# Kernel optimization log

Measured on AMD Instinct MI355X. Metric: run time of the kernel, lower is better.

## Reference

```python
import jax, jax.numpy as jnp
import numpy as np

D_MODEL = 1024
NUM_HEADS = 16
D_K = D_MODEL // NUM_HEADS
THETA = 10000.0
B, S = 2, 2048


def apply_rope(x, token_position, theta=THETA):
    # x: [B, H, S, d_k]; token_position: [B, S] int
    d_k = x.shape[-1]
    inv_freq = 1.0 / theta ** (jnp.arange(0, d_k, 2, dtype=jnp.float32) / d_k)  # [d_k/2]
    angles = token_position.astype(jnp.float32)[:, :, None] * inv_freq[None, None, :]  # [B,S,d_k/2]
    cos = jnp.cos(angles)[:, None, :, :]  # [B,1,S,d_k/2]
    sin = jnp.sin(angles)[:, None, :, :]
    x_even = x[..., 0::2]
    x_odd = x[..., 1::2]
    rot_even = x_even * cos - x_odd * sin
    rot_odd = x_even * sin + x_odd * cos
    # interleave back: stack on new last axis, then flatten
    return jnp.stack([rot_even, rot_odd], axis=-1).reshape(x.shape)


def setup_inputs() -> dict:
    key = jax.random.key(0)
    kx, kq, kk, kv, ko = jax.random.split(key, 5)
    scale = 1.0 / np.sqrt(D_MODEL)
    x = jax.random.normal(kx, (B, S, D_MODEL), dtype=jnp.float32)
    WQ = jax.random.normal(kq, (D_MODEL, D_MODEL), dtype=jnp.float32) * scale
    WK = jax.random.normal(kk, (D_MODEL, D_MODEL), dtype=jnp.float32) * scale
    WV = jax.random.normal(kv, (D_MODEL, D_MODEL), dtype=jnp.float32) * scale
    WO = jax.random.normal(ko, (D_MODEL, D_MODEL), dtype=jnp.float32) * scale
    token_position = jnp.broadcast_to(jnp.arange(S, dtype=jnp.int32)[None, :], (B, S))
    return {"x": x, "token_position": token_position, "WQ": WQ, "WK": WK, "WV": WV, "WO": WO}


def reference(x, token_position, WQ, WK, WV, WO):
    Batch, seq, _ = x.shape
    Q = jnp.einsum('bsd,de->bse', x, WQ).reshape(Batch, seq, NUM_HEADS, D_K).transpose(0, 2, 1, 3)
    K = jnp.einsum('bsd,de->bse', x, WK).reshape(Batch, seq, NUM_HEADS, D_K).transpose(0, 2, 1, 3)
    V = jnp.einsum('bsd,de->bse', x, WV).reshape(Batch, seq, NUM_HEADS, D_K).transpose(0, 2, 1, 3)
    Q = apply_rope(Q, token_position)
    K = apply_rope(K, token_position)
    score = jnp.einsum('bhqd,bhkd->bhqk', Q, K) / jnp.sqrt(jnp.float32(D_K))
    causal = jnp.tril(jnp.ones((seq, seq), dtype=bool))  # [S,S]
    score = jnp.where(causal[None, None, :, :], score, -jnp.inf)
    probs = jax.nn.softmax(score, axis=-1)
    out = jnp.einsum('bhqk,bhkd->bhqd', probs, V)
    out = out.transpose(0, 2, 1, 3).reshape(Batch, seq, D_MODEL)
    return jnp.einsum('bsd,de->bse', out, WO)
```

## Files before the change

kernel.cpp:

```cpp
#include <hip/hip_runtime.h>
#include <hip/hip_bf16.h>

typedef __attribute__((ext_vector_type(8))) short short8;
typedef __attribute__((ext_vector_type(4))) float f32x4;
typedef __hip_bfloat16 bf16_t;

#define SEQ 2048
#define DM 1024
#define NH 16
#define DK 64
#define NKT 16

static __device__ __forceinline__ f32x4 mfma16x16x32(short8 a, short8 b, f32x4 c) {
  return __builtin_amdgcn_mfma_f32_16x16x32_bf16(a, b, c, 0, 0, 0);
}

typedef const __attribute__((address_space(1))) unsigned int ga_u32_t;
typedef __attribute__((address_space(3))) unsigned int lds_u32_t;
static __device__ __forceinline__ void gld16(const bf16_t* g, bf16_t* l) {
  __builtin_amdgcn_global_load_lds((ga_u32_t*)g, (lds_u32_t*)l, 16, 0, 0);
}
static __device__ __forceinline__ void bar() { asm volatile("s_barrier" ::: "memory"); }
static __device__ __forceinline__ void wait_vm8() { asm volatile("s_waitcnt vmcnt(8)" ::: "memory"); }
static __device__ __forceinline__ void wait_vm0() { asm volatile("s_waitcnt vmcnt(0)" ::: "memory"); }

static __device__ __forceinline__ void stage_tile(const bf16_t* asrc, const bf16_t* bsrc,
                                                  char* bufbase, int w, int kk) {
#pragma unroll
  for (int j = 0; j < 4; ++j) {
    gld16(asrc + (size_t)(j * 32) * DM + kk, (bf16_t*)(bufbase + j * 4096 + w * 1024));
    gld16(bsrc + (size_t)(j * 32) * DM + kk, (bf16_t*)(bufbase + 16384 + j * 4096 + w * 1024));
  }
}

__global__ void sniff_dtype(const unsigned int* __restrict__ x, int* __restrict__ flag) {
  int lane = threadIdx.x & 63;
  int cnt = 0;
  for (int r = 0; r < 4; ++r) {
    unsigned int v = x[lane + r * 64];
    int e = (v >> 7) & 0xFF;
    if (e >= 100 && e <= 145) cnt++;
  }
  for (int d = 1; d < 64; d <<= 1) cnt += __shfl_xor(cnt, d, 64);
  if (lane == 0) *flag = (cnt >= 192) ? 1 : 0;
}

__global__ __launch_bounds__(256) void prep(const void* __restrict__ x,
                                            bf16_t* __restrict__ Xc,
                                            const void* __restrict__ w0,
                                            const void* __restrict__ w1,
                                            const void* __restrict__ w2,
                                            const void* __restrict__ w3,
                                            bf16_t* __restrict__ wt_base,
                                            const int* __restrict__ tokpos,
                                            float2* __restrict__ rtab,
                                            const int* __restrict__ flag) {
  int f = *flag;
  int bx = blockIdx.x, t = threadIdx.x;
  __shared__ bf16_t tile[64][65];
  if (bx < 4096) {
    int i = bx * 256 + t;
    if (f) {
      ((uint2*)Xc)[i] = ((const uint2*)x)[i];
    } else {
      const float4 v = ((const float4*)x)[i];
      bf16_t o[4] = {__float2bfloat16(v.x), __float2bfloat16(v.y),
                     __float2bfloat16(v.z), __float2bfloat16(v.w)};
      ((uint2*)Xc)[i] = *(const uint2*)o;
    }
  } else if (bx < 5120) {
    int rem = bx - 4096;
    int z = rem >> 8, bxx = rem & 15, byy = (rem >> 4) & 15;
    const void* src = (z == 0) ? w0 : (z == 1) ? w1 : (z == 2) ? w2 : w3;
    bf16_t* dst = wt_base + (size_t)((z + 1) & 3) * DM * DM;
    int tx = t & 63, ty = t >> 6;
    int r0 = byy * 64, c0 = bxx * 64;
    for (int i = 0; i < 64; i += 4) {
      size_t idx = (size_t)(r0 + ty + i) * DM + c0 + tx;
      tile[ty + i][tx] = f ? ((const bf16_t*)src)[idx]
                           : __float2bfloat16(((const float*)src)[idx]);
    }
    __syncthreads();
    for (int i = 0; i < 64; i += 4)
      dst[(size_t)(c0 + ty + i) * DM + r0 + tx] = tile[tx][ty + i];
  } else {
    int i = (bx - 5120) * 256 + t;
    int m = i >> 5, pp = i & 31;
    float pos = (float)tokpos[m];
    float invf = __powf(10000.0f, -(float)pp * (1.0f / 32.0f));
    float sn, cs;
    sincosf(pos * invf, &sn, &cs);
    rtab[i] = make_float2(cs, sn);
  }
}

__global__ __launch_bounds__(256) void gemm128_qkv(const bf16_t* __restrict__ A,
                                                   const bf16_t* __restrict__ WTqkv,
                                                   bf16_t* __restrict__ Qb,
                                                   bf16_t* __restrict__ Kb,
                                                   bf16_t* __restrict__ VTo,
                                                   const float2* __restrict__ rtab) {
  __shared__ __align__(16) char smem[65536];
  int t = threadIdx.x;
  int w = t >> 6, lane = t & 63, l15 = lane & 15, quad = lane >> 4;
  int wrow = w >> 1, wcol = w & 1;
  int m0 = blockIdx.y * 128, nx = blockIdx.x, n0 = nx * 128;
  int srow0 = w * 8 + (lane >> 3);
  int scg = (lane & 7) ^ (lane >> 3);
  const bf16_t* asrc = A + (size_t)(m0 + srow0) * DM + scg * 8;
  const bf16_t* bsrc = WTqkv + (size_t)(n0 + srow0) * DM + scg * 8;

  f32x4 acc[4][4] = {};
  stage_tile(asrc, bsrc, smem, w, 0);
  stage_tile(asrc, bsrc, smem + 32768, w, 64);
  for (int kt = 0; kt < NKT; ++kt) {
    if (kt < NKT - 1) wait_vm8(); else wait_vm0();
    bar();
    const bf16_t* Ab = (const bf16_t*)(smem + (kt & 1) * 32768);
    const bf16_t* Bb = Ab + 8192;
    short8 af[4][2], bfr[4][2];
#pragma unroll
    for (int mt = 0; mt < 4; ++mt) {
      int r = wrow * 64 + mt * 16 + l15;
      af[mt][0] = *(const short8*)(Ab + r * 64 + ((quad ^ (l15 & 7)) * 8));
      af[mt][1] = *(const short8*)(Ab + r * 64 + (((4 + quad) ^ (l15 & 7)) * 8));
    }
#pragma unroll
    for (int nt = 0; nt < 4; ++nt) {
      int r = wcol * 64 + nt * 16 + l15;
      bfr[nt][0] = *(const short8*)(Bb + r * 64 + ((quad ^ (l15 & 7)) * 8));
      bfr[nt][1] = *(const short8*)(Bb + r * 64 + (((4 + quad) ^ (l15 & 7)) * 8));
    }
#pragma unroll
    for (int mt = 0; mt < 4; ++mt)
#pragma unroll
      for (int nt = 0; nt < 4; ++nt) {
        acc[mt][nt] = mfma16x16x32(af[mt][0], bfr[nt][0], acc[mt][nt]);
        acc[mt][nt] = mfma16x16x32(af[mt][1], bfr[nt][1], acc[mt][nt]);
      }
    bar();
    if (kt + 2 < NKT)
      stage_tile(asrc, bsrc, smem + (kt & 1) * 32768, w, (kt + 2) * 64);
  }

  int sel = nx >> 3;
  int nc = (nx & 7) * 128;
  __syncthreads();
  bf16_t (*Tw)[72] = (bf16_t(*)[72])(smem + w * 9216);
  int b = m0 >> 11;
  int h = (nc >> 6) + wcol;
  if (sel < 2) {
    bf16_t* dst = sel ? Kb : Qb;
    float sgnv = (l15 & 1) ? 1.0f : -1.0f;
#pragma unroll
    for (int mt = 0; mt < 4; ++mt)
#pragma unroll
      for (int r = 0; r < 4; ++r) {
        int m = m0 + wrow * 64 + mt * 16 + quad * 4 + r;
        const float2* tr = rtab + m * 32;
#pragma unroll
        for (int nt = 0; nt < 4; ++nt) {
          int d = nt * 16 + l15;
          float val = acc[mt][nt][r];
          float partner = __shfl_xor(val, 1, 64);
          float2 cssn = tr[d >> 1];
          Tw[mt * 16 + quad * 4 + r][d] = __float2bfloat16(val * cssn.x + sgnv * partner * cssn.y);
        }
      }
    int s_base = (m0 & (SEQ - 1)) + wrow * 64;
    bf16_t* dq = dst + ((size_t)(b * NH + h) * SEQ + s_base) * DK;
#pragma unroll
    for (int c = 0; c < 8; ++c) {
      int row = c * 8 + (lane >> 3);
      int col = (lane & 7) * 8;
      *(short8*)&dq[(size_t)row * DK + col] = *(const short8*)&Tw[row][col];
    }
  } else {
#pragma unroll
    for (int mt = 0; mt < 4; ++mt)
#pragma unroll
      for (int nt = 0; nt < 4; ++nt)
#pragma unroll
        for (int r = 0; r < 4; ++r)
          Tw[nt * 16 + l15][mt * 16 + quad * 4 + r] = __float2bfloat16(acc[mt][nt][r]);
    int s_base = m0 & (SEQ - 1);
#pragma unroll
    for (int c = 0; c < 4; ++c) {
      int d = c * 16 + (lane >> 2);
      int s2 = (lane & 3) * 16;
      size_t ob = ((size_t)(b * NH + h) * DK + d) * SEQ + s_base + wrow * 64 + s2;
      *(short8*)&VTo[ob] = *(const short8*)&Tw[d][s2];
      *(short8*)&VTo[ob + 8] = *(const short8*)&Tw[d][s2 + 8];
    }
  }
}

__global__ __launch_bounds__(256) void gemm128_out(const bf16_t* __restrict__ A,
                                                   const bf16_t* __restrict__ BT,
                                                   void* __restrict__ out,
                                                   const int* __restrict__ flag) {
  __shared__ __align__(16) char smem[65536];
  int f = *flag;
  int t = threadIdx.x;
  int w = t >> 6, lane = t & 63, l15 = lane & 15, quad = lane >> 4;
  int wrow = w >> 1, wcol = w & 1;
  int m0 = blockIdx.y * 128, n0 = blockIdx.x * 128;
  int srow0 = w * 8 + (lane >> 3);
  int scg = (lane & 7) ^ (lane >> 3);
  const bf16_t* asrc = A + (size_t)(m0 + srow0) * DM + scg * 8;
  const bf16_t* bsrc = BT + (size_t)(n0 + srow0) * DM + scg * 8;

  f32x4 acc[4][4] = {};
  stage_tile(asrc, bsrc, smem, w, 0);
  stage_tile(asrc, bsrc, smem + 32768, w, 64);
  for (int kt = 0; kt < NKT; ++kt) {
    if (kt < NKT - 1) wait_vm8(); else wait_vm0();
    bar();
    const bf16_t* Ab = (const bf16_t*)(smem + (kt & 1) * 32768);
    const bf16_t* Bb = Ab + 8192;
    short8 af[4][2], bfr[4][2];
#pragma unroll
    for (int mt = 0; mt < 4; ++mt) {
      int r = wrow * 64 + mt * 16 + l15;
      af[mt][0] = *(const short8*)(Ab + r * 64 + ((quad ^ (l15 & 7)) * 8));
      af[mt][1] = *(const short8*)(Ab + r * 64 + (((4 + quad) ^ (l15 & 7)) * 8));
    }
#pragma unroll
    for (int nt = 0; nt < 4; ++nt) {
      int r = wcol * 64 + nt * 16 + l15;
      bfr[nt][0] = *(const short8*)(Bb + r * 64 + ((quad ^ (l15 & 7)) * 8));
      bfr[nt][1] = *(const short8*)(Bb + r * 64 + (((4 + quad) ^ (l15 & 7)) * 8));
    }
#pragma unroll
    for (int mt = 0; mt < 4; ++mt)
#pragma unroll
      for (int nt = 0; nt < 4; ++nt) {
        acc[mt][nt] = mfma16x16x32(af[mt][0], bfr[nt][0], acc[mt][nt]);
        acc[mt][nt] = mfma16x16x32(af[mt][1], bfr[nt][1], acc[mt][nt]);
      }
    bar();
    if (kt + 2 < NKT)
      stage_tile(asrc, bsrc, smem + (kt & 1) * 32768, w, (kt + 2) * 64);
  }
#pragma unroll
  for (int mt = 0; mt < 4; ++mt)
#pragma unroll
    for (int nt = 0; nt < 4; ++nt)
#pragma unroll
      for (int r = 0; r < 4; ++r) {
        int m = m0 + wrow * 64 + mt * 16 + quad * 4 + r;
        int col = n0 + wcol * 64 + nt * 16 + l15;
        size_t oidx = (size_t)m * DM + col;
        if (f) ((bf16_t*)out)[oidx] = __float2bfloat16(acc[mt][nt][r]);
        else   ((float*)out)[oidx] = acc[mt][nt][r];
      }
}

__global__ __launch_bounds__(256) void attn_fwd(const bf16_t* __restrict__ Q,
                                                const bf16_t* __restrict__ K,
                                                const bf16_t* __restrict__ VT,
                                                bf16_t* __restrict__ O) {
  int x = blockIdx.x, bh = blockIdx.y;
  int b = bh >> 4, h = bh & 15;
  int g = x + (bh << 4);
  int raw = (g + (g >> 8)) & 15;
  const int pmap[16] = {0, 15, 1, 13, 2, 12, 3, 11, 4, 10, 5, 9, 6, 8, 7, 14};
  int p = pmap[raw];
  int qA = p, qB = 31 - p;
  int t = threadIdx.x;
  int w = t >> 6, lane = t & 63, l15 = lane & 15, quad = lane >> 4;
  const size_t base = (size_t)bh * SEQ * DK;
  const bf16_t* Qp = Q + base;
  const bf16_t* Kp = K + base;
  const bf16_t* VTp = VT + base;

  __shared__ __align__(16) bf16_t Ks[64][72];
  __shared__ __align__(16) bf16_t Vs[64][72];
  __shared__ __align__(16) bf16_t Pb[4][2][16][72];

  int rowA = qA * 64 + w * 16 + l15;
  int rowB = qB * 64 + w * 16 + l15;
  short8 qfA0 = *(const short8*)(Qp + (size_t)rowA * DK + quad * 8);
  short8 qfA1 = *(const short8*)(Qp + (size_t)rowA * DK + 32 + quad * 8);
  short8 qfB0 = *(const short8*)(Qp + (size_t)rowB * DK + quad * 8);
  short8 qfB1 = *(const short8*)(Qp + (size_t)rowB * DK + 32 + quad * 8);

  int srow = t >> 2, scoff = (t & 3) * 16;
  const bf16_t* kst = Kp + (size_t)srow * DK + scoff;
  const bf16_t* vst = VTp + (size_t)srow * SEQ + scoff;

  short8 kA = *(const short8*)(kst);
  short8 kB = *(const short8*)(kst + 8);
  short8 vA = *(const short8*)(vst);
  short8 vB = *(const short8*)(vst + 8);

  f32x4 oA[4] = {}, oB[4] = {};
  float rA[4] = {0.f, 0.f, 0.f, 0.f}, rB[4] = {0.f, 0.f, 0.f, 0.f};

  for (int kb = 0; kb <= qB; ++kb) {
    __syncthreads();
    *(short8*)&Ks[srow][scoff] = kA;
    *(short8*)&Ks[srow][scoff + 8] = kB;
    *(short8*)&Vs[srow][scoff] = vA;
    *(short8*)&Vs[srow][scoff + 8] = vB;
    __syncthreads();

    int nkb = (kb < qB) ? (kb + 1) : qB;
    kA = *(const short8*)(kst + (size_t)nkb * 64 * DK);
    kB = *(const short8*)(kst + (size_t)nkb * 64 * DK + 8);
    vA = *(const short8*)(vst + (size_t)nkb * 64);
    vB = *(const short8*)(vst + (size_t)nkb * 64 + 8);

    bool doA = (kb <= qA);

    {
      f32x4 sc[4];
#pragma unroll
      for (int kt = 0; kt < 4; ++kt) {
        f32x4 a = {};
        a = mfma16x16x32(qfB0, *(const short8*)&Ks[kt * 16 + l15][quad * 8], a);
        a = mfma16x16x32(qfB1, *(const short8*)&Ks[kt * 16 + l15][32 + quad * 8], a);
        sc[kt] = a;
      }
      bool diag = (kb == qB);
#pragma unroll
      for (int kt = 0; kt < 4; ++kt)
#pragma unroll
        for (int reg = 0; reg < 4; ++reg) {
          float sv = sc[kt][reg] * 0.125f;
          if (diag) {
            int kg = kt * 16 + l15, qg = w * 16 + quad * 4 + reg;
            if (kg > qg) sv = -30000.0f;
          }
          float pp = __expf(sv);
          rB[reg] += pp;
          Pb[w][1][quad * 4 + reg][kt * 16 + l15] = __float2bfloat16(pp);
        }
      short8 p0 = *(const short8*)&Pb[w][1][l15][quad * 8];
      short8 p1 = *(const short8*)&Pb[w][1][l15][32 + quad * 8];
#pragma unroll
      for (int dt = 0; dt < 4; ++dt) {
        oB[dt] = mfma16x16x32(p0, *(const short8*)&Vs[dt * 16 + l15][quad * 8], oB[dt]);
        oB[dt] = mfma16x16x32(p1, *(const short8*)&Vs[dt * 16 + l15][32 + quad * 8], oB[dt]);
      }
    }
    if (doA) {
      f32x4 sc[4];
#pragma unroll
      for (int kt = 0; kt < 4; ++kt) {
        f32x4 a = {};
        a = mfma16x16x32(qfA0, *(const short8*)&Ks[kt * 16 + l15][quad * 8], a);
        a = mfma16x16x32(qfA1, *(const short8*)&Ks[kt * 16 + l15][32 + quad * 8], a);
        sc[kt] = a;
      }
      bool diag = (kb == qA);
#pragma unroll
      for (int kt = 0; kt < 4; ++kt)
#pragma unroll
        for (int reg = 0; reg < 4; ++reg) {
          float sv = sc[kt][reg] * 0.125f;
          if (diag) {
            int kg = kt * 16 + l15, qg = w * 16 + quad * 4 + reg;
            if (kg > qg) sv = -30000.0f;
          }
          float pp = __expf(sv);
          rA[reg] += pp;
          Pb[w][0][quad * 4 + reg][kt * 16 + l15] = __float2bfloat16(pp);
        }
      short8 p0 = *(const short8*)&Pb[w][0][l15][quad * 8];
      short8 p1 = *(const short8*)&Pb[w][0][l15][32 + quad * 8];
#pragma unroll
      for (int dt = 0; dt < 4; ++dt) {
        oA[dt] = mfma16x16x32(p0, *(const short8*)&Vs[dt * 16 + l15][quad * 8], oA[dt]);
        oA[dt] = mfma16x16x32(p1, *(const short8*)&Vs[dt * 16 + l15][32 + quad * 8], oA[dt]);
      }
    }
  }

  for (int d = 1; d < 16; d <<= 1)
#pragma unroll
    for (int reg = 0; reg < 4; ++reg) {
      rA[reg] += __shfl_xor(rA[reg], d, 64);
      rB[reg] += __shfl_xor(rB[reg], d, 64);
    }

#pragma unroll
  for (int dt = 0; dt < 4; ++dt)
#pragma unroll
    for (int reg = 0; reg < 4; ++reg) {
      int col = h * DK + dt * 16 + l15;
      int qa = qA * 64 + w * 16 + quad * 4 + reg;
      int qb_ = qB * 64 + w * 16 + quad * 4 + reg;
      O[((size_t)b * SEQ + qa) * DM + col] = __float2bfloat16(oA[dt][reg] / rA[reg]);
      O[((size_t)b * SEQ + qb_) * DM + col] = __float2bfloat16(oB[dt][reg] / rB[reg]);
    }
}

extern "C" void kernel_launch(void* const* d_in, const int* in_sizes, int n_in,
                              void* d_out, int out_size, void* d_ws, size_t ws_size,
                              hipStream_t stream) {
  const void* x = d_in[0];
  const int* tokpos = (const int*)d_in[1];
  const void* WQ = d_in[2];
  const void* WK = d_in[3];
  const void* WV = d_in[4];
  const void* WO = d_in[5];

  char* ws = (char*)d_ws;
  const size_t MB = 1024 * 1024;
  bf16_t* WT  = (bf16_t*)ws;
  bf16_t* Xc  = (bf16_t*)(ws + 8 * MB);
  bf16_t* Qb  = (bf16_t*)(ws + 16 * MB);
  bf16_t* Kb  = (bf16_t*)(ws + 24 * MB);
  bf16_t* VTb = (bf16_t*)(ws + 32 * MB);
  bf16_t* Ab  = (bf16_t*)(ws + 8 * MB);
  int* flag   = (int*)(ws + 40 * MB);
  float2* rtab = (float2*)(ws + 41 * MB);

  dim3 blk(256);
  sniff_dtype<<<1, 64, 0, stream>>>((const unsigned int*)x, flag);
  prep<<<5632, blk, 0, stream>>>(x, Xc, WQ, WK, WV, WO, WT, tokpos, rtab, flag);
  gemm128_qkv<<<dim3(24, 32), blk, 0, stream>>>(Xc, WT + (size_t)DM * DM, Qb, Kb, VTb, rtab);
  attn_fwd<<<dim3(16, 32), blk, 0, stream>>>(Qb, Kb, VTb, Ab);
  gemm128_out<<<dim3(8, 32), blk, 0, stream>>>(Ab, WT, d_out, flag);
}
```

Baseline: 185.8 us.

## Split attention KV loop across two wave groups and reduce partials in LDS

Doubles the attention block to 512 threads, with two groups of four waves each handling alternating key blocks (even/odd) for the same query tiles, each group using its own K/V LDS buffers. Partial outputs and row sums from group 1 are written to shared memory and added by group 0 before normalisation and store. This aims to halve the serial KV loop length per block and raise wave-level parallelism. The cost is more LDS (72KB), extra barriers and a final reduction, plus possible idle waves when the count of key blocks is odd.

```diff
diff --git a/kernel.cpp b/kernel.cpp
--- a/kernel.cpp
+++ b/kernel.cpp
@@ -256,70 +256,81 @@
       }
 }
 
-__global__ __launch_bounds__(256) void attn_fwd(const bf16_t* __restrict__ Q,
+__global__ __launch_bounds__(512) void attn_fwd(const bf16_t* __restrict__ Q,
                                                 const bf16_t* __restrict__ K,
                                                 const bf16_t* __restrict__ VT,
                                                 bf16_t* __restrict__ O) {
   int x = blockIdx.x, bh = blockIdx.y;
   int b = bh >> 4, h = bh & 15;
-  int g = x + (bh << 4);
-  int raw = (g + (g >> 8)) & 15;
+  int g4 = x + (bh << 4);
+  int raw = (g4 + (g4 >> 8)) & 15;
   const int pmap[16] = {0, 15, 1, 13, 2, 12, 3, 11, 4, 10, 5, 9, 6, 8, 7, 14};
   int p = pmap[raw];
   int qA = p, qB = 31 - p;
   int t = threadIdx.x;
   int w = t >> 6, lane = t & 63, l15 = lane & 15, quad = lane >> 4;
+  int g = w >> 2;
+  int wq = w & 3;
   const size_t base = (size_t)bh * SEQ * DK;
   const bf16_t* Qp = Q + base;
   const bf16_t* Kp = K + base;
   const bf16_t* VTp = VT + base;
 
-  __shared__ __align__(16) bf16_t Ks[64][72];
-  __shared__ __align__(16) bf16_t Vs[64][72];
-  __shared__ __align__(16) bf16_t Pb[4][2][16][72];
-
-  int rowA = qA * 64 + w * 16 + l15;
-  int rowB = qB * 64 + w * 16 + l15;
+  __shared__ __align__(16) char smem[73728];
+  bf16_t (*Ks)[64][72] = (bf16_t(*)[64][72])smem;
+  bf16_t (*Vs)[64][72] = (bf16_t(*)[64][72])(smem + 18432);
+  bf16_t (*Pb)[2][16][72] = (bf16_t(*)[2][16][72])(smem + 36864);
+
+  int rowA = qA * 64 + wq * 16 + l15;
+  int rowB = qB * 64 + wq * 16 + l15;
   short8 qfA0 = *(const short8*)(Qp + (size_t)rowA * DK + quad * 8);
   short8 qfA1 = *(const short8*)(Qp + (size_t)rowA * DK + 32 + quad * 8);
   short8 qfB0 = *(const short8*)(Qp + (size_t)rowB * DK + quad * 8);
   short8 qfB1 = *(const short8*)(Qp + (size_t)rowB * DK + 32 + quad * 8);
 
-  int srow = t >> 2, scoff = (t & 3) * 16;
+  int tl = t & 255;
+  int srow = tl >> 2, scoff = (tl & 3) * 16;
   const bf16_t* kst = Kp + (size_t)srow * DK + scoff;
   const bf16_t* vst = VTp + (size_t)srow * SEQ + scoff;
 
-  short8 kA = *(const short8*)(kst);
-  short8 kB = *(const short8*)(kst + 8);
-  short8 vA = *(const short8*)(vst);
-  short8 vB = *(const short8*)(vst + 8);
+  short8 kA = *(const short8*)(kst + (size_t)g * 64 * DK);
+  short8 kB = *(const short8*)(kst + (size_t)g * 64 * DK + 8);
+  short8 vA = *(const short8*)(vst + (size_t)g * 64);
+  short8 vB = *(const short8*)(vst + (size_t)g * 64 + 8);
 
   f32x4 oA[4] = {}, oB[4] = {};
   float rA[4] = {0.f, 0.f, 0.f, 0.f}, rB[4] = {0.f, 0.f, 0.f, 0.f};
 
-  for (int kb = 0; kb <= qB; ++kb) {
+  int ni = qB / 2 + 1;
+  for (int i = 0; i < ni; ++i) {
+    int kb = 2 * i + g;
+    bool active = (kb <= qB);
     __syncthreads();
-    *(short8*)&Ks[srow][scoff] = kA;
-    *(short8*)&Ks[srow][scoff + 8] = kB;
-    *(short8*)&Vs[srow][scoff] = vA;
-    *(short8*)&Vs[srow][scoff + 8] = vB;
+    if (active) {
+      *(short8*)&Ks[g][srow][scoff] = kA;
+      *(short8*)&Ks[g][srow][scoff + 8] = kB;
+      *(short8*)&Vs[g][srow][scoff] = vA;
+      *(short8*)&Vs[g][srow][scoff + 8] = vB;
+    }
     __syncthreads();
 
-    int nkb = (kb < qB) ? (kb + 1) : qB;
-    kA = *(const short8*)(kst + (size_t)nkb * 64 * DK);
-    kB = *(const short8*)(kst + (size_t)nkb * 64 * DK + 8);
-    vA = *(const short8*)(vst + (size_t)nkb * 64);
-    vB = *(const short8*)(vst + (size_t)nkb * 64 + 8);
+    int nkb = (kb + 2 <= qB) ? (kb + 2) : kb;
+    if (active) {
+      kA = *(const short8*)(kst + (size_t)nkb * 64 * DK);
+      kB = *(const short8*)(kst + (size_t)nkb * 64 * DK + 8);
+      vA = *(const short8*)(vst + (size_t)nkb * 64);
+      vB = *(const short8*)(vst + (size_t)nkb * 64 + 8);
+    }
+    if (!active) continue;
 
     bool doA = (kb <= qA);
-
     {
       f32x4 sc[4];
 #pragma unroll
       for (int kt = 0; kt < 4; ++kt) {
         f32x4 a = {};
-        a = mfma16x16x32(qfB0, *(const short8*)&Ks[kt * 16 + l15][quad * 8], a);
-        a = mfma16x16x32(qfB1, *(const short8*)&Ks[kt * 16 + l15][32 + quad * 8], a);
+        a = mfma16x16x32(qfB0, *(const short8*)&Ks[g][kt * 16 + l15][quad * 8], a);
+        a = mfma16x16x32(qfB1, *(const short8*)&Ks[g][kt * 16 + l15][32 + quad * 8], a);
         sc[kt] = a;
       }
       bool diag = (kb == qB);
@@ -329,7 +340,7 @@
         for (int reg = 0; reg < 4; ++reg) {
           float sv = sc[kt][reg] * 0.125f;
           if (diag) {
-            int kg = kt * 16 + l15, qg = w * 16 + quad * 4 + reg;
+            int kg = kt * 16 + l15, qg = wq * 16 + quad * 4 + reg;
             if (kg > qg) sv = -30000.0f;
           }
           float pp = __expf(sv);
@@ -340,8 +351,8 @@
       short8 p1 = *(const short8*)&Pb[w][1][l15][32 + quad * 8];
 #pragma unroll
       for (int dt = 0; dt < 4; ++dt) {
-        oB[dt] = mfma16x16x32(p0, *(const short8*)&Vs[dt * 16 + l15][quad * 8], oB[dt]);
-        oB[dt] = mfma16x16x32(p1, *(const short8*)&Vs[dt * 16 + l15][32 + quad * 8], oB[dt]);
+        oB[dt] = mfma16x16x32(p0, *(const short8*)&Vs[g][dt * 16 + l15][quad * 8], oB[dt]);
+        oB[dt] = mfma16x16x32(p1, *(const short8*)&Vs[g][dt * 16 + l15][32 + quad * 8], oB[dt]);
       }
     }
     if (doA) {
@@ -349,8 +360,8 @@
 #pragma unroll
       for (int kt = 0; kt < 4; ++kt) {
         f32x4 a = {};
-        a = mfma16x16x32(qfA0, *(const short8*)&Ks[kt * 16 + l15][quad * 8], a);
-        a = mfma16x16x32(qfA1, *(const short8*)&Ks[kt * 16 + l15][32 + quad * 8], a);
+        a = mfma16x16x32(qfA0, *(const short8*)&Ks[g][kt * 16 + l15][quad * 8], a);
+        a = mfma16x16x32(qfA1, *(const short8*)&Ks[g][kt * 16 + l15][32 + quad * 8], a);
         sc[kt] = a;
       }
       bool diag = (kb == qA);
@@ -360,7 +371,7 @@
         for (int reg = 0; reg < 4; ++reg) {
           float sv = sc[kt][reg] * 0.125f;
           if (diag) {
-            int kg = kt * 16 + l15, qg = w * 16 + quad * 4 + reg;
+            int kg = kt * 16 + l15, qg = wq * 16 + quad * 4 + reg;
             if (kg > qg) sv = -30000.0f;
           }
           float pp = __expf(sv);
@@ -371,8 +382,8 @@
       short8 p1 = *(const short8*)&Pb[w][0][l15][32 + quad * 8];
 #pragma unroll
       for (int dt = 0; dt < 4; ++dt) {
-        oA[dt] = mfma16x16x32(p0, *(const short8*)&Vs[dt * 16 + l15][quad * 8], oA[dt]);
-        oA[dt] = mfma16x16x32(p1, *(const short8*)&Vs[dt * 16 + l15][32 + quad * 8], oA[dt]);
+        oA[dt] = mfma16x16x32(p0, *(const short8*)&Vs[g][dt * 16 + l15][quad * 8], oA[dt]);
+        oA[dt] = mfma16x16x32(p1, *(const short8*)&Vs[g][dt * 16 + l15][32 + quad * 8], oA[dt]);
       }
     }
   }
@@ -384,16 +395,51 @@
       rB[reg] += __shfl_xor(rB[reg], d, 64);
     }
 
-#pragma unroll
-  for (int dt = 0; dt < 4; ++dt)
+  float (*OcA)[16][68] = (float(*)[16][68])smem;
+  float (*OcB)[16][68] = (float(*)[16][68])(smem + 17408);
+  float (*RcA)[16] = (float(*)[16])(smem + 34816);
+  float (*RcB)[16] = (float(*)[16])(smem + 35072);
+  __syncthreads();
+  if (g == 1) {
+#pragma unroll
+    for (int dt = 0; dt < 4; ++dt)
+#pragma unroll
+      for (int reg = 0; reg < 4; ++reg) {
+        OcA[wq][quad * 4 + reg][dt * 16 + l15] = oA[dt][reg];
+        OcB[wq][quad * 4 + reg][dt * 16 + l15] = oB[dt][reg];
+      }
+    if (l15 == 0)
+#pragma unroll
+      for (int reg = 0; reg < 4; ++reg) {
+        RcA[wq][quad * 4 + reg] = rA[reg];
+        RcB[wq][quad * 4 + reg] = rB[reg];
+      }
+  }
+  __syncthreads();
+  if (g == 0) {
+#pragma unroll
+    for (int dt = 0; dt < 4; ++dt)
+#pragma unroll
+      for (int reg = 0; reg < 4; ++reg) {
+        oA[dt][reg] += OcA[wq][quad * 4 + reg][dt * 16 + l15];
+        oB[dt][reg] += OcB[wq][quad * 4 + reg][dt * 16 + l15];
+      }
 #pragma unroll
     for (int reg = 0; reg < 4; ++reg) {
-      int col = h * DK + dt * 16 + l15;
-      int qa = qA * 64 + w * 16 + quad * 4 + reg;
-      int qb_ = qB * 64 + w * 16 + quad * 4 + reg;
-      O[((size_t)b * SEQ + qa) * DM + col] = __float2bfloat16(oA[dt][reg] / rA[reg]);
-      O[((size_t)b * SEQ + qb_) * DM + col] = __float2bfloat16(oB[dt][reg] / rB[reg]);
-    }
+      rA[reg] += RcA[wq][quad * 4 + reg];
+      rB[reg] += RcB[wq][quad * 4 + reg];
+    }
+#pragma unroll
+    for (int dt = 0; dt < 4; ++dt)
+#pragma unroll
+      for (int reg = 0; reg < 4; ++reg) {
+        int col = h * DK + dt * 16 + l15;
+        int qa = qA * 64 + wq * 16 + quad * 4 + reg;
+        int qb_ = qB * 64 + wq * 16 + quad * 4 + reg;
+        O[((size_t)b * SEQ + qa) * DM + col] = __float2bfloat16(oA[dt][reg] / rA[reg]);
+        O[((size_t)b * SEQ + qb_) * DM + col] = __float2bfloat16(oB[dt][reg] / rB[reg]);
+      }
+  }
 }
 
 extern "C" void kernel_launch(void* const* d_in, const int* in_sizes, int n_in,
@@ -418,9 +464,10 @@
   float2* rtab = (float2*)(ws + 41 * MB);
 
   dim3 blk(256);
+  dim3 blk512(512);
   sniff_dtype<<<1, 64, 0, stream>>>((const unsigned int*)x, flag);
   prep<<<5632, blk, 0, stream>>>(x, Xc, WQ, WK, WV, WO, WT, tokpos, rtab, flag);
   gemm128_qkv<<<dim3(24, 32), blk, 0, stream>>>(Xc, WT + (size_t)DM * DM, Qb, Kb, VTb, rtab);
-  attn_fwd<<<dim3(16, 32), blk, 0, stream>>>(Qb, Kb, VTb, Ab);
+  attn_fwd<<<dim3(16, 32), blk512, 0, stream>>>(Qb, Kb, VTb, Ab);
   gemm128_out<<<dim3(8, 32), blk, 0, stream>>>(Ab, WT, d_out, flag);
 }
```

Result: no change. 189.1 us (+1.8%).
